# Performance work log

Measured on AMD Instinct MI355X. Metric: run time of the kernel, lower is better.

Reference implementation:

```python
import jax, jax.numpy as jnp
import numpy as np
from jax import lax

B, N, C, T = 32, 1000, 32, 24
K, F_CHEB, F_TIME = 3, 64, 64


def setup_inputs() -> dict:
    key = jax.random.key(0)
    ks = jax.random.split(key, 7)
    return {
        "x": jax.random.normal(ks[0], (B, N, C, T), dtype=jnp.float32),
        "cheb_T": jax.random.normal(ks[1], (K, N, N), dtype=jnp.float32) * (1.0 / np.sqrt(N)),
        "Theta": jax.random.normal(ks[2], (K, C, F_CHEB), dtype=jnp.float32) * 0.1,
        "time_w": jax.random.normal(ks[3], (F_TIME, F_CHEB, 1, 3), dtype=jnp.float32) * 0.05,
        "time_b": jax.random.normal(ks[4], (F_TIME,), dtype=jnp.float32) * 0.05,
        "res_w": jax.random.normal(ks[5], (F_TIME, C, 1, 1), dtype=jnp.float32) * 0.1,
        "res_b": jax.random.normal(ks[6], (F_TIME,), dtype=jnp.float32) * 0.05,
    }


def _conv2d(x, w, stride_t, pad_t):
    # x: [B, Cin, N, T] (NCHW with H=nodes, W=time), w: [Cout, Cin, kh, kw]
    return lax.conv_general_dilated(
        x, w, window_strides=(1, stride_t), padding=((0, 0), (pad_t, pad_t)),
        dimension_numbers=("NCHW", "OIHW", "NCHW"))


def reference(x, cheb_T, Theta, time_w, time_b, res_w, res_b):
    # ChebConv: rhs_k[b,n,c,t] = sum_m T_k[m,n] x[b,m,c,t]; out = sum_k rhs_k @ Theta_k
    # Fused over all timesteps and polynomial orders in one einsum.
    spatial = jax.nn.relu(
        jnp.einsum("knm,bmct,kcf->bnft", cheb_T, x, Theta))  # [B,N,F_cheb,T]
    # time conv over the T axis (kernel (1,3), pad (0,1), stride (1,1))
    h = spatial.transpose(0, 2, 1, 3)  # [B,F_cheb,N,T]
    tc = _conv2d(h, time_w, 1, 1) + time_b[None, :, None, None]
    tc = jnp.tanh(tc) * jax.nn.sigmoid(tc)  # wave-net gating
    # 1x1 residual conv on the raw input (Dropout output in source is unused)
    res = _conv2d(x.transpose(0, 2, 1, 3), res_w, 1, 0) + res_b[None, :, None, None]
    out = (res + tc).transpose(0, 2, 1, 3)  # [B,N,F_time,T]
    return out
```

## Files before the change

kernel.cpp:

```cpp
#include <hip/hip_runtime.h>
#include <math.h>

typedef __attribute__((ext_vector_type(4))) float f32x4;
typedef __attribute__((ext_vector_type(8))) short s16x8;
typedef __attribute__((ext_vector_type(8))) unsigned short u16x8;
typedef __attribute__((ext_vector_type(4))) unsigned short u16x4;

#define NB 32
#define NN 1000
#define NT 24
#define NP 1024
#define TCN 768

#define GLOAD16(g, l) __builtin_amdgcn_global_load_lds( \
    (const __attribute__((address_space(1))) unsigned int*)(g), \
    (__attribute__((address_space(3))) unsigned int*)(l), 16, 0, 0)

__device__ __forceinline__ unsigned short f2bf(float f){
  union { float fv; unsigned int u; } v; v.fv = f;
  unsigned int r = v.u + 0x7FFFu + ((v.u >> 16) & 1u);
  return (unsigned short)(r >> 16);
}

__global__ void k0_cheb(const float* __restrict__ cheb, unsigned short* __restrict__ cbT){
  int idx = blockIdx.x * 256 + threadIdx.x;
  int base = idx << 2;
  int m = base & (NP - 1);
  int r = base >> 10;
  int n = r & (NP - 1);
  int k = r >> 10;
  u16x4 o;
  #pragma unroll
  for (int i = 0; i < 4; ++i){
    int mm = m + i;
    float v = (n < NN && mm < NN) ? cheb[((long)k*NN + n)*NN + mm] : 0.f;
    o[i] = f2bf(v);
  }
  *(u16x4*)(cbT + base) = o;
}

__global__ __launch_bounds__(256) void k0_x(const float* __restrict__ x,
                     unsigned short* __restrict__ xbT, unsigned short* __restrict__ xt2){
  __shared__ unsigned short tile[64*770];
  const int b  = blockIdx.x >> 4;
  const int m0 = (blockIdx.x & 15) << 6;
  const int tid = threadIdx.x;
  for (int i = tid; i < 64*192; i += 256){
    int mi = i / 192, c4 = (i - mi*192) << 2;
    f32x4 v = (f32x4){0.f,0.f,0.f,0.f};
    if (m0 + mi < NN) v = *(const f32x4*)(x + (size_t)(b*NN + m0 + mi)*768 + c4);
    unsigned short* tp = tile + mi*770 + c4;
    tp[0] = f2bf(v[0]); tp[1] = f2bf(v[1]); tp[2] = f2bf(v[2]); tp[3] = f2bf(v[3]);
  }
  __syncthreads();
  {
    const int seg = tid & 7, r0 = tid >> 3;
    for (int rr = 0; rr < 768; rr += 32){
      int r = rr + r0;
      int t = r >> 5, c = r & 31, ct = c*24 + t;
      u16x8 v;
      #pragma unroll
      for (int e = 0; e < 8; ++e) v[e] = tile[(seg*8 + e)*770 + ct];
      *(u16x8*)(xbT + ((size_t)b*TCN + r)*NP + m0 + seg*8) = v;
    }
  }
  if (m0 < NN){
    int rows = NN - m0; if (rows > 64) rows = 64;
    for (int i = tid; i < rows*96; i += 256){
      int mi = i / 96, s = i - mi*96;
      u16x8 v;
      #pragma unroll
      for (int e = 0; e < 8; ++e){
        int r = s*8 + e; int t = r >> 5, c = r & 31;
        v[e] = tile[mi*770 + c*24 + t];
      }
      *(u16x8*)(xt2 + (size_t)(b*NN + m0 + mi)*TCN + s*8) = v;
    }
  }
}

__global__ void k0_w(const float* __restrict__ Theta, const float* __restrict__ tw,
                     const float* __restrict__ rw,
                     unsigned short* __restrict__ ThT, unsigned short* __restrict__ WtT,
                     unsigned short* __restrict__ rwT){
  int i = blockIdx.x * 256 + threadIdx.x;
  if (i < 64*96){
    int f = i / 96, kc = i - f*96;
    ThT[i] = f2bf(Theta[kc*64 + f]);
  }
  if (i < 64*192){
    int f = i / 192, kk = i - f*192;
    int dt = kk >> 6, fi = kk & 63;
    WtT[i] = f2bf(tw[(f*64 + fi)*3 + dt]);
  }
  if (i < 64*32){
    rwT[i] = f2bf(rw[i]);
  }
}

__global__ __launch_bounds__(512, 4) void k1_cheb_theta(
    const unsigned short* __restrict__ cbT,
    const unsigned short* __restrict__ xbT,
    const unsigned short* __restrict__ ThT,
    unsigned short* __restrict__ spa)
{
  __shared__ __align__(16) unsigned short smem[14336];

  int pB = blockIdx.x;
  int lb = (pB & 7) * 384 + (pB >> 3);
  const int tct = lb % 12; lb /= 12;
  const int nt  = lb & 7;
  const int b   = lb >> 3;

  const int tid  = threadIdx.x;
  const int wid  = tid >> 6;
  const int lane = tid & 63;
  const int l16  = lane & 15;
  const int k8   = lane >> 4;
  const int wr   = wid & 3;
  const int wc   = wid >> 2;

  const int rl4  = lane >> 2;
  const int swz8 = (((lane & 3) ^ ((rl4 >> 1) & 3)) << 3);
  const unsigned short* gA = cbT + (size_t)(nt*128 + rl4)*NP + swz8;
  const unsigned short* gB = xbT + ((size_t)b*TCN + tct*64 + rl4)*NP + swz8;

  const int rdsw = ((k8 ^ ((l16 >> 1) & 3)) << 3);

  f32x4 acc[3][2][2];
  #pragma unroll
  for (int k = 0; k < 3; ++k)
    #pragma unroll
    for (int i = 0; i < 2; ++i)
      #pragma unroll
      for (int j = 0; j < 2; ++j) acc[k][i][j] = (f32x4){0.f, 0.f, 0.f, 0.f};

  for (int step = 0; step < 32; ++step){
    __syncthreads();
    const int so = step << 5;
    #pragma unroll
    for (int q = 0; q < 4; ++q){
      const int g = wid + (q << 3);
      if (g < 24){
        const int k = g >> 3, rg = g & 7;
        GLOAD16(gA + (size_t)k*NP*NP + (size_t)rg*16*NP + so,
                (char*)smem + k*8192 + rg*1024);
      } else if (g < 28){
        const int rg = g - 24;
        GLOAD16(gB + (size_t)rg*16*NP + so,
                (char*)smem + 24576 + rg*1024);
      }
    }
    __syncthreads();
    s16x8 af[3][2], bf[2];
    #pragma unroll
    for (int k = 0; k < 3; ++k)
      #pragma unroll
      for (int i = 0; i < 2; ++i)
        af[k][i] = *(const s16x8*)(smem + k*4096 + (wr*32 + i*16 + l16)*32 + rdsw);
    #pragma unroll
    for (int j = 0; j < 2; ++j)
      bf[j] = *(const s16x8*)(smem + 12288 + (wc*32 + j*16 + l16)*32 + rdsw);
    #pragma unroll
    for (int k = 0; k < 3; ++k)
      #pragma unroll
      for (int i = 0; i < 2; ++i)
        #pragma unroll
        for (int j = 0; j < 2; ++j)
          acc[k][i][j] = __builtin_amdgcn_mfma_f32_16x16x32_bf16(af[k][i], bf[j], acc[k][i][j], 0, 0, 0);
  }

  s16x8 b2[3][4];
  #pragma unroll
  for (int ch = 0; ch < 3; ++ch)
    #pragma unroll
    for (int j = 0; j < 4; ++j)
      b2[ch][j] = *(const s16x8*)(ThT + (j*16 + l16)*96 + ch*32 + k8*8);

  unsigned short* yl = smem;
  #pragma unroll
  for (int p = 0; p < 2; ++p){
    __syncthreads();
    if (wc == p){
      #pragma unroll
      for (int k = 0; k < 3; ++k)
        #pragma unroll
        for (int i = 0; i < 2; ++i)
          #pragma unroll
          for (int j = 0; j < 2; ++j){
            const int nb = wr*32 + i*16 + (k8 << 2);
            #pragma unroll
            for (int r = 0; r < 4; ++r)
              yl[(nb + r)*104 + k*32 + j*16 + l16] = f2bf(acc[k][i][j][r]);
          }
    }
    __syncthreads();
    f32x4 acc2[4];
    #pragma unroll
    for (int j = 0; j < 4; ++j) acc2[j] = (f32x4){0.f,0.f,0.f,0.f};
    #pragma unroll
    for (int ch = 0; ch < 3; ++ch){
      s16x8 a2 = *(const s16x8*)(yl + (size_t)(wid*16 + l16)*104 + ch*32 + k8*8);
      #pragma unroll
      for (int j = 0; j < 4; ++j)
        acc2[j] = __builtin_amdgcn_mfma_f32_16x16x32_bf16(a2, b2[ch][j], acc2[j], 0, 0, 0);
    }
    const int tg = tct*2 + p;
    #pragma unroll
    for (int j = 0; j < 4; ++j)
      #pragma unroll
      for (int r = 0; r < 4; ++r){
        const int n = nt*128 + wid*16 + (k8 << 2) + r;
        if (n < NN)
          spa[((size_t)(b*NN + n)*NT + tg)*64 + j*16 + l16] = f2bf(fmaxf(acc2[j][r], 0.f));
      }
  }
}

__global__ __launch_bounds__(256, 2) void k2_out(
    const unsigned short* __restrict__ spa, const unsigned short* __restrict__ xt2,
    const unsigned short* __restrict__ WtT, const unsigned short* __restrict__ rwT,
    const float* __restrict__ tb, const float* __restrict__ rb,
    float* __restrict__ out)
{
  const int tid  = threadIdx.x;
  const int wid  = tid >> 6;
  const int lane = tid & 63;
  const int l16  = lane & 15;
  const int k8   = lane >> 4;
  const int gwave = blockIdx.x * 4 + wid;

  s16x8 bw[6][4], br[4];
  #pragma unroll
  for (int ch = 0; ch < 6; ++ch)
    #pragma unroll
    for (int j = 0; j < 4; ++j)
      bw[ch][j] = *(const s16x8*)(WtT + (j*16 + l16)*192 + ch*32 + k8*8);
  #pragma unroll
  for (int j = 0; j < 4; ++j)
    br[j] = *(const s16x8*)(rwT + (j*16 + l16)*32 + k8*8);
  float tbv[4], rbv[4];
  #pragma unroll
  for (int j = 0; j < 4; ++j){ tbv[j] = tb[j*16 + l16]; rbv[j] = rb[j*16 + l16]; }

  for (int it = 0; it < 8; ++it){
    const int r0 = (gwave*8 + it) * 16;
    const int rowA = r0 + l16;
    const int tA = rowA % 24;
    const int bn = rowA / 24;
    f32x4 acc_tc[4], acc_res[4];
    #pragma unroll
    for (int j = 0; j < 4; ++j){ acc_tc[j] = (f32x4){0.f,0.f,0.f,0.f}; acc_res[j] = (f32x4){0.f,0.f,0.f,0.f}; }

    #pragma unroll
    for (int ch = 0; ch < 6; ++ch){
      const int dt = ch >> 1, fh = (ch & 1) << 5;
      const int ts = tA + dt - 1;
      s16x8 a = (s16x8){0,0,0,0,0,0,0,0};
      if (ts >= 0 && ts < 24)
        a = *(const s16x8*)(spa + ((size_t)(bn*24 + ts) << 6) + fh + k8*8);
      #pragma unroll
      for (int j = 0; j < 4; ++j)
        acc_tc[j] = __builtin_amdgcn_mfma_f32_16x16x32_bf16(a, bw[ch][j], acc_tc[j], 0, 0, 0);
    }
    {
      s16x8 a = *(const s16x8*)(xt2 + (size_t)bn*768 + tA*32 + k8*8);
      #pragma unroll
      for (int j = 0; j < 4; ++j)
        acc_res[j] = __builtin_amdgcn_mfma_f32_16x16x32_bf16(a, br[j], acc_res[j], 0, 0, 0);
    }

    const int rowD = r0 + (k8 << 2);
    const int tD  = rowD % 24;
    const int bnD = rowD / 24;
    #pragma unroll
    for (int j = 0; j < 4; ++j){
      f32x4 v;
      #pragma unroll
      for (int r = 0; r < 4; ++r){
        float z = acc_tc[j][r] + tbv[j];
        float e = __expf(-z);
        float p = (1.f - e) * __builtin_amdgcn_rcpf(1.f + e*e);
        v[r] = acc_res[j][r] + rbv[j] + p;
      }
      *(f32x4*)(out + (((size_t)bnD << 6) + j*16 + l16)*24 + tD) = v;
    }
  }
}

extern "C" void kernel_launch(void* const* d_in, const int* in_sizes, int n_in,
                              void* d_out, int out_size, void* d_ws, size_t ws_size,
                              hipStream_t stream) {
  const float* x     = (const float*)d_in[0];
  const float* cheb  = (const float*)d_in[1];
  const float* Theta = (const float*)d_in[2];
  const float* tw    = (const float*)d_in[3];
  const float* tb    = (const float*)d_in[4];
  const float* rw    = (const float*)d_in[5];
  const float* rb    = (const float*)d_in[6];
  float* out = (float*)d_out;

  char* ws = (char*)d_ws;
  size_t off = 0;
  auto alloc = [&](size_t bytes) -> void* {
    void* p = ws + off;
    off += (bytes + 255) & ~(size_t)255;
    return p;
  };
  unsigned short* cbT = (unsigned short*)alloc((size_t)3*NP*NP*2);
  unsigned short* xbT = (unsigned short*)alloc((size_t)NB*TCN*NP*2);
  unsigned short* xt2 = (unsigned short*)alloc((size_t)NB*NN*TCN*2);
  unsigned short* spa = (unsigned short*)alloc((size_t)NB*NN*NT*64*2);
  unsigned short* ThT = (unsigned short*)alloc((size_t)64*96*2);
  unsigned short* WtT = (unsigned short*)alloc((size_t)64*192*2);
  unsigned short* rwT = (unsigned short*)alloc((size_t)64*32*2);

  hipLaunchKernelGGL(k0_cheb, dim3(3072), dim3(256), 0, stream, cheb, cbT);
  hipLaunchKernelGGL(k0_x,    dim3(512),  dim3(256), 0, stream, x, xbT, xt2);
  hipLaunchKernelGGL(k0_w,    dim3(48),   dim3(256), 0, stream, Theta, tw, rw, ThT, WtT, rwT);
  hipLaunchKernelGGL(k1_cheb_theta, dim3(32*8*12), dim3(512), 0, stream, cbT, xbT, ThT, spa);
  hipLaunchKernelGGL(k2_out,  dim3(1500), dim3(256), 0, stream, spa, xt2, WtT, rwT, tb, rb, out);
}
```

Measured before the change: 457.5 us.

## Double-buffer Chebyshev GEMM, switch to 32x32 MFMA tiles, retile k1 and k2

Rewrites the Chebyshev GEMM kernel to use 256-thread blocks with a 64-node by 128-column tile. It double-buffers the LDS k-slices, so the next slice's global-to-LDS load is issued while MFMAs run on the current one, and it uses 32x32x16 bf16 MFMA instead of 16x16x32. The Theta epilogue is reworked for the new layout with an XOR-swizzled LDS staging buffer. k2 now does half the rows per wave over twice as many blocks. The intent is to hide load latency and remove one barrier per step. The cost is more LDS per block and a larger accumulator register footprint, which may limit occupancy.

```diff
diff --git a/kernel.cpp b/kernel.cpp
--- a/kernel.cpp
+++ b/kernel.cpp
@@ -2,6 +2,7 @@
 #include <math.h>
 
 typedef __attribute__((ext_vector_type(4))) float f32x4;
+typedef __attribute__((ext_vector_type(16))) float f32x16;
 typedef __attribute__((ext_vector_type(8))) short s16x8;
 typedef __attribute__((ext_vector_type(8))) unsigned short u16x8;
 typedef __attribute__((ext_vector_type(4))) unsigned short u16x4;
@@ -98,126 +99,146 @@
   }
 }
 
-__global__ __launch_bounds__(512, 4) void k1_cheb_theta(
+__global__ __launch_bounds__(256, 3) void k1_cheb_theta(
     const unsigned short* __restrict__ cbT,
     const unsigned short* __restrict__ xbT,
     const unsigned short* __restrict__ ThT,
     unsigned short* __restrict__ spa)
 {
-  __shared__ __align__(16) unsigned short smem[14336];
+  __shared__ __align__(16) unsigned short smem[20480];
 
   int pB = blockIdx.x;
   int lb = (pB & 7) * 384 + (pB >> 3);
-  const int tct = lb % 12; lb /= 12;
-  const int nt  = lb & 7;
-  const int b   = lb >> 3;
+  const int tcb = lb % 6; lb /= 6;
+  const int nt  = lb & 15;
+  const int b   = lb >> 4;
 
   const int tid  = threadIdx.x;
   const int wid  = tid >> 6;
   const int lane = tid & 63;
-  const int l16  = lane & 15;
-  const int k8   = lane >> 4;
-  const int wr   = wid & 3;
-  const int wc   = wid >> 2;
-
-  const int rl4  = lane >> 2;
-  const int swz8 = (((lane & 3) ^ ((rl4 >> 1) & 3)) << 3);
-  const unsigned short* gA = cbT + (size_t)(nt*128 + rl4)*NP + swz8;
-  const unsigned short* gB = xbT + ((size_t)b*TCN + tct*64 + rl4)*NP + swz8;
-
-  const int rdsw = ((k8 ^ ((l16 >> 1) & 3)) << 3);
-
-  f32x4 acc[3][2][2];
+  const int l31  = lane & 31;
+  const int h    = lane >> 5;
+  const int wr   = wid >> 1;
+  const int wc   = wid & 1;
+
+  const int rl4 = lane >> 2;
+  const int swz = (((lane & 3) ^ (rl4 & 3)) << 3);
+  const unsigned short* baseA = cbT + (size_t)(nt*64 + rl4)*NP + swz;
+  const unsigned short* baseB = xbT + ((size_t)b*TCN + tcb*128 + rl4)*NP + swz;
+  char* smc = (char*)smem;
+
+  const int ch0 = ((h ^ (lane & 3)) << 3);
+  const int ch1 = (((2 + h) ^ (lane & 3)) << 3);
+
+  f32x16 acc[3][2];
   #pragma unroll
   for (int k = 0; k < 3; ++k)
     #pragma unroll
-    for (int i = 0; i < 2; ++i)
-      #pragma unroll
-      for (int j = 0; j < 2; ++j) acc[k][i][j] = (f32x4){0.f, 0.f, 0.f, 0.f};
-
+    for (int j = 0; j < 2; ++j)
+      #pragma unroll
+      for (int r = 0; r < 16; ++r) acc[k][j][r] = 0.f;
+
+  const int rA  = wr*32 + l31;
+  const int rB0 = wc*64 + l31;
+
+  {
+    #pragma unroll
+    for (int q = 0; q < 5; ++q){
+      const int g = wid*5 + q;
+      if (g < 12){
+        const int k = g >> 2, rg = g & 3;
+        GLOAD16(baseA + (size_t)k*NP*NP + rg*16*NP, smc + k*4096 + rg*1024);
+      } else {
+        const int rg = g - 12;
+        GLOAD16(baseB + (size_t)rg*16*NP, smc + 12288 + rg*1024);
+      }
+    }
+  }
+  __syncthreads();
+
+  int cur = 0;
   for (int step = 0; step < 32; ++step){
+    if (step < 31){
+      const int so = (step + 1) << 5;
+      const int bo = (cur ^ 1) * 20480;
+      #pragma unroll
+      for (int q = 0; q < 5; ++q){
+        const int g = wid*5 + q;
+        if (g < 12){
+          const int k = g >> 2, rg = g & 3;
+          GLOAD16(baseA + (size_t)k*NP*NP + rg*16*NP + so, smc + bo + k*4096 + rg*1024);
+        } else {
+          const int rg = g - 12;
+          GLOAD16(baseB + (size_t)rg*16*NP + so, smc + bo + 12288 + rg*1024);
+        }
+      }
+    }
+    const unsigned short* sb = smem + cur*10240;
+    #pragma unroll
+    for (int ks = 0; ks < 2; ++ks){
+      const int ch = ks ? ch1 : ch0;
+      s16x8 bf0 = *(const s16x8*)(sb + 6144 + rB0*32 + ch);
+      s16x8 bf1 = *(const s16x8*)(sb + 6144 + (rB0 + 32)*32 + ch);
+      #pragma unroll
+      for (int k = 0; k < 3; ++k){
+        s16x8 af = *(const s16x8*)(sb + k*2048 + rA*32 + ch);
+        acc[k][0] = __builtin_amdgcn_mfma_f32_32x32x16_bf16(af, bf0, acc[k][0], 0, 0, 0);
+        acc[k][1] = __builtin_amdgcn_mfma_f32_32x32x16_bf16(af, bf1, acc[k][1], 0, 0, 0);
+      }
+    }
     __syncthreads();
-    const int so = step << 5;
-    #pragma unroll
-    for (int q = 0; q < 4; ++q){
-      const int g = wid + (q << 3);
-      if (g < 24){
-        const int k = g >> 3, rg = g & 7;
-        GLOAD16(gA + (size_t)k*NP*NP + (size_t)rg*16*NP + so,
-                (char*)smem + k*8192 + rg*1024);
-      } else if (g < 28){
-        const int rg = g - 24;
-        GLOAD16(gB + (size_t)rg*16*NP + so,
-                (char*)smem + 24576 + rg*1024);
-      }
-    }
+    cur ^= 1;
+  }
+
+  s16x8 b2[3][2];
+  const int fE = wc*32 + l31;
+  #pragma unroll
+  for (int ch = 0; ch < 3; ++ch)
+    #pragma unroll
+    for (int ks = 0; ks < 2; ++ks)
+      b2[ch][ks] = *(const s16x8*)(ThT + fE*96 + ch*32 + ks*16 + h*8);
+
+  unsigned short* yl = smem;
+  const int rowE = wr*32 + l31;
+  #pragma unroll
+  for (int p = 0; p < 4; ++p){
     __syncthreads();
-    s16x8 af[3][2], bf[2];
-    #pragma unroll
-    for (int k = 0; k < 3; ++k)
-      #pragma unroll
-      for (int i = 0; i < 2; ++i)
-        af[k][i] = *(const s16x8*)(smem + k*4096 + (wr*32 + i*16 + l16)*32 + rdsw);
-    #pragma unroll
-    for (int j = 0; j < 2; ++j)
-      bf[j] = *(const s16x8*)(smem + 12288 + (wc*32 + j*16 + l16)*32 + rdsw);
-    #pragma unroll
-    for (int k = 0; k < 3; ++k)
-      #pragma unroll
-      for (int i = 0; i < 2; ++i)
-        #pragma unroll
-        for (int j = 0; j < 2; ++j)
-          acc[k][i][j] = __builtin_amdgcn_mfma_f32_16x16x32_bf16(af[k][i], bf[j], acc[k][i][j], 0, 0, 0);
-  }
-
-  s16x8 b2[3][4];
-  #pragma unroll
-  for (int ch = 0; ch < 3; ++ch)
-    #pragma unroll
-    for (int j = 0; j < 4; ++j)
-      b2[ch][j] = *(const s16x8*)(ThT + (j*16 + l16)*96 + ch*32 + k8*8);
-
-  unsigned short* yl = smem;
-  #pragma unroll
-  for (int p = 0; p < 2; ++p){
-    __syncthreads();
-    if (wc == p){
+    if (wc == (p >> 1)){
+      const int jj = p & 1;
       #pragma unroll
       for (int k = 0; k < 3; ++k)
         #pragma unroll
-        for (int i = 0; i < 2; ++i)
-          #pragma unroll
-          for (int j = 0; j < 2; ++j){
-            const int nb = wr*32 + i*16 + (k8 << 2);
-            #pragma unroll
-            for (int r = 0; r < 4; ++r)
-              yl[(nb + r)*104 + k*32 + j*16 + l16] = f2bf(acc[k][i][j][r]);
-          }
+        for (int r = 0; r < 16; ++r){
+          const int nl = wr*32 + (r & 3) + ((r >> 2) << 3) + (h << 2);
+          const int kc = k*32 + l31;
+          const int q  = kc >> 3;
+          yl[nl*104 + (((q ^ (nl & 3)) << 3) | (kc & 7))] = f2bf(acc[k][jj][r]);
+        }
     }
     __syncthreads();
-    f32x4 acc2[4];
-    #pragma unroll
-    for (int j = 0; j < 4; ++j) acc2[j] = (f32x4){0.f,0.f,0.f,0.f};
-    #pragma unroll
-    for (int ch = 0; ch < 3; ++ch){
-      s16x8 a2 = *(const s16x8*)(yl + (size_t)(wid*16 + l16)*104 + ch*32 + k8*8);
-      #pragma unroll
-      for (int j = 0; j < 4; ++j)
-        acc2[j] = __builtin_amdgcn_mfma_f32_16x16x32_bf16(a2, b2[ch][j], acc2[j], 0, 0, 0);
-    }
-    const int tg = tct*2 + p;
-    #pragma unroll
-    for (int j = 0; j < 4; ++j)
-      #pragma unroll
-      for (int r = 0; r < 4; ++r){
-        const int n = nt*128 + wid*16 + (k8 << 2) + r;
-        if (n < NN)
-          spa[((size_t)(b*NN + n)*NT + tg)*64 + j*16 + l16] = f2bf(fmaxf(acc2[j][r], 0.f));
-      }
-  }
-}
-
-__global__ __launch_bounds__(256, 2) void k2_out(
+    f32x16 a2c;
+    #pragma unroll
+    for (int r = 0; r < 16; ++r) a2c[r] = 0.f;
+    #pragma unroll
+    for (int ch = 0; ch < 3; ++ch)
+      #pragma unroll
+      for (int ks = 0; ks < 2; ++ks){
+        const int q = ch*4 + ks*2 + h;
+        s16x8 a2 = *(const s16x8*)(yl + rowE*104 + ((q ^ (rowE & 3)) << 3));
+        a2c = __builtin_amdgcn_mfma_f32_32x32x16_bf16(a2, b2[ch][ks], a2c, 0, 0, 0);
+      }
+    const int t = tcb*4 + p;
+    #pragma unroll
+    for (int r = 0; r < 16; ++r){
+      const int nl = wr*32 + (r & 3) + ((r >> 2) << 3) + (h << 2);
+      const int n  = nt*64 + nl;
+      if (n < NN)
+        spa[((size_t)(b*NN + n)*NT + t)*64 + fE] = f2bf(fmaxf(a2c[r], 0.f));
+    }
+  }
+}
+
+__global__ __launch_bounds__(256, 3) void k2_out(
     const unsigned short* __restrict__ spa, const unsigned short* __restrict__ xt2,
     const unsigned short* __restrict__ WtT, const unsigned short* __restrict__ rwT,
     const float* __restrict__ tb, const float* __restrict__ rb,
@@ -243,8 +264,8 @@
   #pragma unroll
   for (int j = 0; j < 4; ++j){ tbv[j] = tb[j*16 + l16]; rbv[j] = rb[j*16 + l16]; }
 
-  for (int it = 0; it < 8; ++it){
-    const int r0 = (gwave*8 + it) * 16;
+  for (int it = 0; it < 4; ++it){
+    const int r0 = gwave*64 + it*16;
     const int rowA = r0 + l16;
     const int tA = rowA % 24;
     const int bn = rowA / 24;
@@ -318,6 +339,6 @@
   hipLaunchKernelGGL(k0_cheb, dim3(3072), dim3(256), 0, stream, cheb, cbT);
   hipLaunchKernelGGL(k0_x,    dim3(512),  dim3(256), 0, stream, x, xbT, xt2);
   hipLaunchKernelGGL(k0_w,    dim3(48),   dim3(256), 0, stream, Theta, tw, rw, ThT, WtT, rwT);
-  hipLaunchKernelGGL(k1_cheb_theta, dim3(32*8*12), dim3(512), 0, stream, cbT, xbT, ThT, spa);
-  hipLaunchKernelGGL(k2_out,  dim3(1500), dim3(256), 0, stream, spa, xt2, WtT, rwT, tb, rb, out);
-}
+  hipLaunchKernelGGL(k1_cheb_theta, dim3(32*16*6), dim3(256), 0, stream, cbT, xbT, ThT, spa);
+  hipLaunchKernelGGL(k2_out,  dim3(3000), dim3(256), 0, stream, spa, xt2, WtT, rwT, tb, rb, out);
+}
```

Measured after the change: 443.6 us. 1.03x faster.
